# Kernel tuning notes

Measured on AMD Instinct MI355X. Metric: run time of the kernel, lower is better.

The kernel has to match this reference:

```python
import jax, jax.numpy as jnp
import numpy as np

N_HEADS = 8
LN_EPS = 1e-5
NEG = -1e9


def _layernorm(x, g, b):
    mu = jnp.mean(x, axis=-1, keepdims=True)
    var = jnp.var(x, axis=-1, keepdims=True)
    return (x - mu) * jax.lax.rsqrt(var + LN_EPS) * g + b


def setup_inputs() -> dict:
    key = jax.random.key(0)
    ks = jax.random.split(key, 16)
    B, T, D, W, L, A = 8, 256, 512, 32, 4, 6
    s = 0.02
    return {
        "feats": jax.random.normal(ks[0], (B, T, D), jnp.float32),
        "pos_embed": jax.random.normal(ks[1], (1, W, D), jnp.float32) * s,
        "Wqkv": jax.random.normal(ks[2], (L, 3 * D, D), jnp.float32) * s,
        "bqkv": jnp.zeros((L, 3 * D), jnp.float32),
        "Wo": jax.random.normal(ks[3], (L, D, D), jnp.float32) * s,
        "bo": jnp.zeros((L, D), jnp.float32),
        "ln1_g": jnp.ones((L, D), jnp.float32),
        "ln1_b": jnp.zeros((L, D), jnp.float32),
        "W1": jax.random.normal(ks[4], (L, 4 * D, D), jnp.float32) * s,
        "b1": jnp.zeros((L, 4 * D), jnp.float32),
        "W2": jax.random.normal(ks[5], (L, D, 4 * D), jnp.float32) * s,
        "b2": jnp.zeros((L, D), jnp.float32),
        "ln2_g": jnp.ones((L, D), jnp.float32),
        "ln2_b": jnp.zeros((L, D), jnp.float32),
        "Wp": jax.random.normal(ks[6], (A, D), jnp.float32) * s,
        "bp": jnp.zeros((A,), jnp.float32),
        "Wv": jax.random.normal(ks[7], (1, D), jnp.float32) * s,
        "bv": jnp.zeros((1,), jnp.float32),
    }


def reference(feats, pos_embed, Wqkv, bqkv, Wo, bo, ln1_g, ln1_b,
              W1, b1, W2, b2, ln2_g, ln2_b, Wp, bp, Wv, bv):
    B, T, D = feats.shape
    W = pos_embed.shape[1]
    L = Wqkv.shape[0]
    H = N_HEADS
    dh = D // H

    # Sliding windows for every timestep t: window slot w holds frame
    # max(t+1-W+w, 0)  (left-pad short prefixes by repeating frame 0).
    idx = jnp.maximum(jnp.arange(T)[:, None] + 1 - W + jnp.arange(W)[None, :], 0)  # (T,W)
    x = feats[:, idx, :].reshape(B * T, W, D) + pos_embed  # (B*T, W, D)

    causal = jnp.tril(jnp.ones((W, W), bool))  # additive -inf upper-tri mask

    for i in range(L):
        qkv = x @ Wqkv[i].T + bqkv[i]                     # (N,W,3D)
        q, k, v = jnp.split(qkv, 3, axis=-1)
        q = q.reshape(-1, W, H, dh).transpose(0, 2, 1, 3)
        k = k.reshape(-1, W, H, dh).transpose(0, 2, 1, 3)
        v = v.reshape(-1, W, H, dh).transpose(0, 2, 1, 3)
        scores = jnp.einsum('nhqd,nhkd->nhqk', q, k) / jnp.sqrt(jnp.float32(dh))
        scores = jnp.where(causal, scores, NEG)
        attn = jax.nn.softmax(scores, axis=-1)
        ctx = jnp.einsum('nhqk,nhkd->nhqd', attn, v)
        ctx = ctx.transpose(0, 2, 1, 3).reshape(-1, W, D)
        x = _layernorm(x + ctx @ Wo[i].T + bo[i], ln1_g[i], ln1_b[i])
        ff = jax.nn.relu(x @ W1[i].T + b1[i]) @ W2[i].T + b2[i]
        x = _layernorm(x + ff, ln2_g[i], ln2_b[i])

    token = x[:, -1, :].reshape(B, T, D)
    logits = token @ Wp.T + bp          # (B,T,A)
    values = (token @ Wv.T + bv)[..., 0]  # (B,T)
    return logits, values
```

## Files before the change

kernel.cpp:

```cpp
#include <hip/hip_runtime.h>
#include <hip/hip_bf16.h>
#include <cstdint>
#include <cstddef>

#define B_    8
#define T_    256
#define D_    512
#define W_    32
#define L_    4
#define A_    6
#define H_    8
#define DH_   64
#define NWIN  (B_*T_)
#define NTOK  (NWIN*W_)
#define FROWS 2176
#define SMALL (NWIN*D_)

typedef __hip_bfloat16 bf16;
using bf16x8 = __attribute__((ext_vector_type(8))) short;
using f32x4  = __attribute__((ext_vector_type(4))) float;
using f32x16 = __attribute__((ext_vector_type(16))) float;

#define XB_BYTES  ((size_t)NTOK * D_ * 2)
#define WQ_ELEMS  ((size_t)L_ * 3*D_*D_)
#define WO_ELEMS  ((size_t)L_ * D_*D_)
#define W1_ELEMS  ((size_t)L_ * 4*D_*D_)
#define W2_ELEMS  ((size_t)L_ * 4*D_*D_)
#define WB_BYTES  ((WQ_ELEMS + WO_ELEMS + W1_ELEMS + W2_ELEMS) * 2)
#define FB_ELEMS  ((size_t)FROWS * D_)
#define QF_ELEMS  ((size_t)FROWS * 3*D_)
#define SCR_BYTES ((size_t)NTOK * 2560 * 2)
#define TOTAL_BYTES (XB_BYTES + WB_BYTES + (FB_ELEMS + QF_ELEMS)*2 + SCR_BYTES)

static char* g_fallback = nullptr;
__attribute__((constructor)) static void alloc_fallback() {
    (void)hipMalloc((void**)&g_fallback, TOTAL_BYTES);
}

typedef __attribute__((address_space(3))) uint8_t* as3p;
typedef const __attribute__((address_space(1))) uint8_t* as1p;
__device__ __forceinline__ void gload_lds16(const void* g, void* l) {
    __builtin_amdgcn_global_load_lds((as1p)(const uint8_t*)g,
                                     (as3p)(uint32_t)(uintptr_t)l, 16, 0, 0);
}

__device__ __forceinline__ float bf2f(short s) {
    return __uint_as_float(((uint32_t)(uint16_t)s) << 16);
}
__device__ __forceinline__ short f2bf(float f) {
    return (short)__bfloat16_as_ushort(__float2bfloat16(f));
}

__global__ __launch_bounds__(256) void cvt_kernel(
    const float* __restrict__ w, bf16* __restrict__ o, int n4)
{
    int i = blockIdx.x * 256 + threadIdx.x;
    if (i >= n4) return;
    float4 f = ((const float4*)w)[i];
    bf16* d = o + (size_t)i * 4;
    d[0] = __float2bfloat16(f.x);
    d[1] = __float2bfloat16(f.y);
    d[2] = __float2bfloat16(f.z);
    d[3] = __float2bfloat16(f.w);
}

__global__ __launch_bounds__(256) void build_x_kernel(
    const float* __restrict__ feats,
    const float* __restrict__ pos,
    bf16* __restrict__ xb)
{
    int gid   = blockIdx.x * 256 + threadIdx.x;
    int token = gid >> 7;
    int c4    = (gid & 127) * 4;
    int w     = token & (W_-1);
    int n     = token >> 5;
    int t     = n & (T_-1);
    int b     = n >> 8;
    int frame = t + w - (W_-1); if (frame < 0) frame = 0;
    const float4 f = *(const float4*)(feats + ((size_t)(b*T_ + frame)*D_ + c4));
    const float4 p = *(const float4*)(pos   + ((size_t)w*D_ + c4));
    bf16* d = xb + (size_t)token*D_ + c4;
    d[0] = __float2bfloat16(f.x + p.x);
    d[1] = __float2bfloat16(f.y + p.y);
    d[2] = __float2bfloat16(f.z + p.z);
    d[3] = __float2bfloat16(f.w + p.w);
}

__global__ __launch_bounds__(256) void build_fb_kernel(
    const float* __restrict__ feats,
    const float* __restrict__ pos,
    bf16* __restrict__ fb)
{
    int gid = blockIdx.x * 256 + threadIdx.x;
    int row = gid >> 7;
    int c4  = (gid & 127) * 4;
    bf16* d = fb + (size_t)row * D_ + c4;
    float4 f;
    if (row < 2048)      f = *(const float4*)(feats + (size_t)row * D_ + c4);
    else if (row < 2080) f = *(const float4*)(pos + (size_t)(row - 2048) * D_ + c4);
    else                 f = make_float4(0.f, 0.f, 0.f, 0.f);
    d[0] = __float2bfloat16(f.x);
    d[1] = __float2bfloat16(f.y);
    d[2] = __float2bfloat16(f.z);
    d[3] = __float2bfloat16(f.w);
}

__global__ __launch_bounds__(256) void qkv_gather_kernel(
    const bf16* __restrict__ qf,
    const float* __restrict__ bq,
    bf16* __restrict__ qkv)
{
    int gid   = blockIdx.x * 256 + threadIdx.x;
    int token = gid / 192;
    int c0    = (gid % 192) * 8;
    int w     = token & (W_-1);
    int n     = token >> 5;
    int t     = n & (T_-1);
    int b     = n >> 8;
    int frame = t + w - (W_-1); if (frame < 0) frame = 0;
    const bf16x8 a = *(const bf16x8*)(qf + (size_t)(b*T_ + frame) * (3*D_) + c0);
    const bf16x8 p = *(const bf16x8*)(qf + (size_t)(2048 + w)     * (3*D_) + c0);
    bf16x8 o;
#pragma unroll
    for (int j = 0; j < 8; ++j)
        o[j] = f2bf(bf2f(a[j]) + bf2f(p[j]) + bq[c0 + j]);
    *(bf16x8*)(qkv + (size_t)token * (3*D_) + c0) = o;
}

template<bool RELU, bool BIAS, bool REMAP>
__global__ __launch_bounds__(256) void gemm_bf16(
    const bf16* __restrict__ A,
    const bf16* __restrict__ Bt,
    const float* __restrict__ bias,
    bf16* __restrict__ Cb,
    int M, int N, int K)
{
    __shared__ bf16 As[128*32];
    __shared__ bf16 Bs[128*32];

    const int tid  = threadIdx.x;
    const int lane = tid & 63;
    const int wv   = tid >> 6;

    const int gridN = N >> 7;
    const int bid   = blockIdx.x;
    int m0, n0;
    if (REMAP) {
        const int q_ = bid >> 3;
        n0 = (q_ % gridN) << 7;
        m0 = (((q_ / gridN) * 8) + (bid & 7)) << 7;
    } else {
        n0 = (bid % gridN) << 7;
        m0 = (bid / gridN) << 7;
    }

    const int wm = (wv >> 1) * 64;
    const int wn = (wv & 1) * 64;

    f32x16 acc[2][2] = {};

    const int   srow  = wv*16 + (lane >> 2);
    const int   skoff = (lane & 3) * 8;
    const bf16* ga0 = A  + (size_t)(m0 + srow)      * K + skoff;
    const bf16* ga1 = A  + (size_t)(m0 + 64 + srow) * K + skoff;
    const bf16* gb0 = Bt + (size_t)(n0 + srow)      * K + skoff;
    const bf16* gb1 = Bt + (size_t)(n0 + 64 + srow) * K + skoff;
    char* lAs = (char*)As;
    char* lBs = (char*)Bs;
    const int l0 = wv*1024 + lane*16;

    const int r32  = lane & 31;
    const int ksel = (lane >> 5) * 16;

    for (int k0 = 0; k0 < K; k0 += 32) {
        gload_lds16(ga0 + k0, lAs + l0);
        gload_lds16(ga1 + k0, lAs + l0 + 4096);
        gload_lds16(gb0 + k0, lBs + l0);
        gload_lds16(gb1 + k0, lBs + l0 + 4096);
        __syncthreads();

        bf16x8 av[2][2], bv[2][2];
#pragma unroll
        for (int i = 0; i < 2; ++i)
#pragma unroll
            for (int h = 0; h < 2; ++h) {
                av[i][h] = *(const bf16x8*)(lAs + (wm + i*32 + r32)*64 + h*32 + ksel);
                bv[i][h] = *(const bf16x8*)(lBs + (wn + i*32 + r32)*64 + h*32 + ksel);
            }
#pragma unroll
        for (int i = 0; i < 2; ++i)
#pragma unroll
            for (int j = 0; j < 2; ++j) {
                acc[i][j] = __builtin_amdgcn_mfma_f32_32x32x16_bf16(
                    av[i][0], bv[j][0], acc[i][j], 0, 0, 0);
                acc[i][j] = __builtin_amdgcn_mfma_f32_32x32x16_bf16(
                    av[i][1], bv[j][1], acc[i][j], 0, 0, 0);
            }
        __syncthreads();
    }

    const int rbase = (lane >> 5) * 4;
#pragma unroll
    for (int i = 0; i < 2; ++i) {
#pragma unroll
        for (int j = 0; j < 2; ++j) {
            const int ncol = n0 + wn + j*32 + r32;
            const float bv_ = BIAS ? bias[ncol] : 0.f;
#pragma unroll
            for (int reg = 0; reg < 16; ++reg) {
                const int mrow = m0 + wm + i*32 + (reg & 3) + 8*(reg >> 2) + rbase;
                float v = acc[i][j][reg] + bv_;
                if (RELU) v = fmaxf(v, 0.f);
                Cb[(size_t)mrow * N + ncol] = __float2bfloat16(v);
            }
        }
    }
}

template<bool RELU, bool BIAS>
__global__ __launch_bounds__(512, 2) void gemm256(
    const bf16* __restrict__ A,
    const bf16* __restrict__ Bt,
    const float* __restrict__ bias,
    bf16* __restrict__ Cb,
    int M, int N, int K)
{
    (void)M;
    __shared__ bf16 As[2][256*64];
    __shared__ bf16 Bs[2][256*64];

    const int tid  = threadIdx.x;
    const int lane = tid & 63;
    const int wv   = tid >> 6;
    const int wm   = wv >> 2;
    const int wn   = wv & 3;
    const int L    = lane & 15;
    const int qd   = lane >> 4;

    const int gridN = N >> 8;
    const int W8  = gridN << 3;
    const int bid = blockIdx.x;
    const int q_  = bid / W8;
    const int r_  = bid % W8;
    const int n0  = (r_ >> 3) << 8;
    const int m0  = ((q_ << 3) + (r_ & 7)) << 8;

    const int srow = tid >> 3;
    const int scol = ((tid & 7) ^ (srow & 7)) * 8;
    const bf16* gA = A  + (size_t)(m0 + srow) * K + scol;
    const bf16* gB = Bt + (size_t)(n0 + srow) * K + scol;
    const size_t rstep = (size_t)64 * K;
    bf16* lA = &As[0][0] + tid * 8;
    bf16* lB = &Bs[0][0] + tid * 8;

    const int physk0 = ((qd)     ^ (L & 7)) * 8;
    const int physk1 = ((4 + qd) ^ (L & 7)) * 8;
    const int aoff = (wm*128 + L) * 64;
    const int boff = (wn*64  + L) * 64;

    f32x4 acc[8][4] = {};
    bf16x8 av0[4][2], av1[4][2], bv0[2][2], bv1[2][2];

#define STAGE_A2(b, kt) do { \
    const bf16* s_ = gA + (size_t)(kt) * 64; \
    bf16* d_ = lA + (b) * 16384; \
    gload_lds16(s_,            d_); \
    gload_lds16(s_ +   rstep,  d_ + 4096); \
    gload_lds16(s_ + 2*rstep,  d_ + 8192); \
    gload_lds16(s_ + 3*rstep,  d_ + 12288); } while (0)

#define STAGE_B2(b, kt) do { \
    const bf16* s_ = gB + (size_t)(kt) * 64; \
    bf16* d_ = lB + (b) * 16384; \
    gload_lds16(s_,            d_); \
    gload_lds16(s_ +   rstep,  d_ + 4096); \
    gload_lds16(s_ + 2*rstep,  d_ + 8192); \
    gload_lds16(s_ + 3*rstep,  d_ + 12288); } while (0)

#define LDA_(dst, b, qm) do { \
    const bf16* pa_ = &As[b][aoff + (qm)*4096]; \
    _Pragma("unroll") \
    for (int mr_ = 0; mr_ < 4; ++mr_) { \
        dst[mr_][0] = *(const bf16x8*)(pa_ + mr_*1024 + physk0); \
        dst[mr_][1] = *(const bf16x8*)(pa_ + mr_*1024 + physk1); } } while (0)

#define LDB_(dst, b, qn) do { \
    const bf16* pb_ = &Bs[b][boff + (qn)*2048]; \
    _Pragma("unroll") \
    for (int nr_ = 0; nr_ < 2; ++nr_) { \
        dst[nr_][0] = *(const bf16x8*)(pb_ + nr_*1024 + physk0); \
        dst[nr_][1] = *(const bf16x8*)(pb_ + nr_*1024 + physk1); } } while (0)

#define MMA_(qm, qn, av, bv) do { \
    _Pragma("unroll") \
    for (int mr_ = 0; mr_ < 4; ++mr_) \
    _Pragma("unroll") \
    for (int nr_ = 0; nr_ < 2; ++nr_) { \
        f32x4 c_ = acc[(qm)*4+mr_][(qn)*2+nr_]; \
        c_ = __builtin_amdgcn_mfma_f32_16x16x32_bf16(av[mr_][0], bv[nr_][0], c_, 0, 0, 0); \
        c_ = __builtin_amdgcn_mfma_f32_16x16x32_bf16(av[mr_][1], bv[nr_][1], c_, 0, 0, 0); \
        acc[(qm)*4+mr_][(qn)*2+nr_] = c_; } } while (0)

#define BAR_ __builtin_amdgcn_s_barrier()
#define LGKM0_ do { asm volatile("s_waitcnt lgkmcnt(0)" ::: "memory"); \
                    __builtin_amdgcn_sched_barrier(0); } while (0)

#define TILE_(b, kt2) do { \
     \
    LDA_(av0, b, 0); LDB_(bv0, b, 0); \
    BAR_; LGKM0_; \
    __builtin_amdgcn_s_setprio(1); MMA_(0, 0, av0, bv0); __builtin_amdgcn_s_setprio(0); \
    BAR_; \
     \
    LDB_(bv1, b, 1); \
    BAR_; LGKM0_; \
    __builtin_amdgcn_s_setprio(1); MMA_(0, 1, av0, bv1); __builtin_amdgcn_s_setprio(0); \
    BAR_; \
     \
    LDA_(av1, b, 1); \
    STAGE_B2(b, kt2); \
    BAR_; LGKM0_; \
    __builtin_amdgcn_s_setprio(1); MMA_(1, 1, av1, bv1); __builtin_amdgcn_s_setprio(0); \
    BAR_; \
     \
    STAGE_A2(b, kt2); \
    __builtin_amdgcn_s_setprio(1); MMA_(1, 0, av1, bv0); __builtin_amdgcn_s_setprio(0); \
    asm volatile("s_waitcnt vmcnt(8)" ::: "memory"); \
    BAR_; } while (0)

    const int nkt = K >> 6;

    STAGE_B2(0, 0); STAGE_A2(0, 0);
    STAGE_B2(1, 1); STAGE_A2(1, 1);
    asm volatile("s_waitcnt vmcnt(8)" ::: "memory");
    BAR_;

    for (int u = 0; u < nkt; u += 2) {
        int k2 = u + 2; if (k2 >= nkt) k2 -= nkt;
        int k3 = u + 3; if (k3 >= nkt) k3 -= nkt;
        TILE_(0, k2);
        TILE_(1, k3);
    }

    asm volatile("s_waitcnt vmcnt(0)" ::: "memory");

#pragma unroll
    for (int mr = 0; mr < 8; ++mr) {
        const int row = m0 + wm*128 + mr*16 + qd*4;
#pragma unroll
        for (int nr = 0; nr < 4; ++nr) {
            const int col = n0 + wn*64 + nr*16 + L;
            const float bb = BIAS ? bias[col] : 0.f;
            bf16* cp = Cb + (size_t)row * N + col;
#pragma unroll
            for (int rg = 0; rg < 4; ++rg) {
                float v = acc[mr][nr][rg] + bb;
                if (RELU) v = fmaxf(v, 0.f);
                cp[(size_t)rg * N] = __float2bfloat16(v);
            }
        }
    }

#undef STAGE_A2
#undef STAGE_B2
#undef LDA_
#undef LDB_
#undef MMA_
#undef BAR_
#undef LGKM0_
#undef TILE_
}

__global__ __launch_bounds__(256) void lnres_kernel(
    const bf16* __restrict__ y,
    const bf16* __restrict__ xin,
    bf16* __restrict__ xout,
    const float* __restrict__ g,
    const float* __restrict__ b,
    int xin_stride)
{
    const int wave  = threadIdx.x >> 6;
    const int lane  = threadIdx.x & 63;
    const int token = blockIdx.x * 4 + wave;
    const int c0    = lane * 8;

    const bf16* yr = y    + (size_t)token * D_ + c0;
    const bf16* xr = xin  + (size_t)token * xin_stride + c0;
    bf16*       xo = xout + (size_t)token * D_ + c0;

    bf16x8 ty = *(const bf16x8*)yr;
    bf16x8 tx = *(const bf16x8*)xr;

    float v[8];
    float s1 = 0.f, s2 = 0.f;
#pragma unroll
    for (int j = 0; j < 8; ++j) {
        v[j] = bf2f(ty[j]) + bf2f(tx[j]);
        s1 += v[j]; s2 += v[j]*v[j];
    }
#pragma unroll
    for (int mask = 1; mask < 64; mask <<= 1) {
        s1 += __shfl_xor(s1, mask);
        s2 += __shfl_xor(s2, mask);
    }
    const float mu = s1 * (1.f / D_);
    float var = s2 * (1.f / D_) - mu * mu;
    if (var < 0.f) var = 0.f;
    const float rs = rsqrtf(var + 1e-5f);

    const float4 g0 = *(const float4*)(g + c0);
    const float4 g1 = *(const float4*)(g + c0 + 4);
    const float4 b0 = *(const float4*)(b + c0);
    const float4 b1 = *(const float4*)(b + c0 + 4);
    const float gg[8] = {g0.x,g0.y,g0.z,g0.w,g1.x,g1.y,g1.z,g1.w};
    const float bb[8] = {b0.x,b0.y,b0.z,b0.w,b1.x,b1.y,b1.z,b1.w};

    bf16x8 o;
#pragma unroll
    for (int j = 0; j < 8; ++j) {
        float t = (v[j] - mu) * rs * gg[j] + bb[j];
        o[j] = f2bf(t);
    }
    *(bf16x8*)xo = o;
}

__global__ __launch_bounds__(256) void attn_mfma(
    const bf16* __restrict__ qkv,
    bf16* __restrict__ ctx)
{
    __shared__ short Pb[4][32*32];

    const int tid  = threadIdx.x;
    const int lane = tid & 63;
    const int wv   = tid >> 6;
    const int pair = blockIdx.x * 4 + wv;
    const int win  = pair >> 3;
    const int h    = pair & 7;

    const int quad = lane >> 4;
    const int col  = lane & 15;

    const bf16* base = qkv + (size_t)win * W_ * (3*D_) + h * DH_;

    bf16x8 bvv[4];
    {
        const short* vbase = (const short*)(base + 2*D_);
#pragma unroll
        for (int ntd = 0; ntd < 4; ++ntd)
#pragma unroll
            for (int jj = 0; jj < 8; ++jj)
                bvv[ntd][jj] = vbase[(size_t)(quad*8 + jj) * (3*D_) + ntd*16 + col];
    }

    bf16x8 aq[2][2], bk[2][2];
#pragma unroll
    for (int mt = 0; mt < 2; ++mt)
#pragma unroll
        for (int kq = 0; kq < 2; ++kq)
            aq[mt][kq] = *(const bf16x8*)(base + (size_t)(mt*16 + col) * (3*D_)
                                          + kq*32 + quad*8);
#pragma unroll
    for (int nt = 0; nt < 2; ++nt)
#pragma unroll
        for (int kq = 0; kq < 2; ++kq)
            bk[nt][kq] = *(const bf16x8*)(base + D_ + (size_t)(nt*16 + col) * (3*D_)
                                          + kq*32 + quad*8);

    f32x4 S[2][2] = {};
#pragma unroll
    for (int mt = 0; mt < 2; ++mt)
#pragma unroll
        for (int nt = 0; nt < 2; ++nt) {
            S[mt][nt] = __builtin_amdgcn_mfma_f32_16x16x32_bf16(
                aq[mt][0], bk[nt][0], S[mt][nt], 0, 0, 0);
            S[mt][nt] = __builtin_amdgcn_mfma_f32_16x16x32_bf16(
                aq[mt][1], bk[nt][1], S[mt][nt], 0, 0, 0);
        }

    short* P = Pb[wv];
#pragma unroll
    for (int mt = 0; mt < 2; ++mt) {
#pragma unroll
        for (int reg = 0; reg < 4; ++reg) {
            const int row = mt*16 + quad*4 + reg;
            float v0 = (col      <= row) ? S[mt][0][reg] * 0.125f : -1e30f;
            float v1 = (16 + col <= row) ? S[mt][1][reg] * 0.125f : -1e30f;
            float mx = fmaxf(v0, v1);
#pragma unroll
            for (int m = 1; m < 16; m <<= 1) mx = fmaxf(mx, __shfl_xor(mx, m));
            float e0 = __expf(v0 - mx);
            float e1 = __expf(v1 - mx);
            float sm = e0 + e1;
#pragma unroll
            for (int m = 1; m < 16; m <<= 1) sm += __shfl_xor(sm, m);
            float inv = 1.f / sm;
            P[row*32 + col]      = f2bf(e0 * inv);
            P[row*32 + 16 + col] = f2bf(e1 * inv);
        }
    }

    bf16* cb = ctx + (size_t)win * W_ * D_ + h * DH_;
#pragma unroll
    for (int mt = 0; mt < 2; ++mt) {
        bf16x8 ap = *(const bf16x8*)(P + (mt*16 + col)*32 + quad*8);
#pragma unroll
        for (int ntd = 0; ntd < 4; ++ntd) {
            f32x4 O = {};
            O = __builtin_amdgcn_mfma_f32_16x16x32_bf16(ap, bvv[ntd], O, 0, 0, 0);
#pragma unroll
            for (int reg = 0; reg < 4; ++reg) {
                const int row = mt*16 + quad*4 + reg;
                cb[(size_t)row * D_ + ntd*16 + col] = __float2bfloat16(O[reg]);
            }
        }
    }
}

__global__ __launch_bounds__(256) void attn_last(
    const bf16* __restrict__ qkv,
    bf16* __restrict__ ctxl)
{
    __shared__ float Ps[4][32];

    const int wv   = threadIdx.x >> 6;
    const int lane = threadIdx.x & 63;
    const int pair = blockIdx.x * 4 + wv;
    const int win  = pair >> 3;
    const int h    = pair & 7;

    const bf16* base = qkv + (size_t)win * W_ * (3*D_) + h * DH_;
    const short* qrow = (const short*)(base + (size_t)(W_-1) * (3*D_));

    const int k    = lane & 31;
    const int half = lane >> 5;
    const short* krow = (const short*)(base + D_ + (size_t)k * (3*D_) + half*32);

    float s = 0.f;
    const bf16x8* q8 = (const bf16x8*)(qrow + half*32);
    const bf16x8* k8 = (const bf16x8*)krow;
#pragma unroll
    for (int c = 0; c < 4; ++c) {
        bf16x8 qa = q8[c], kb = k8[c];
#pragma unroll
        for (int j = 0; j < 8; ++j) s += bf2f(qa[j]) * bf2f(kb[j]);
    }
    s += __shfl_xor(s, 32);
    s *= 0.125f;

    float mx = s;
#pragma unroll
    for (int m = 1; m < 32; m <<= 1) mx = fmaxf(mx, __shfl_xor(mx, m));
    float e = __expf(s - mx);
    float sum = e;
#pragma unroll
    for (int m = 1; m < 32; m <<= 1) sum += __shfl_xor(sum, m);
    if (half == 0) Ps[wv][k] = e / sum;
    __syncthreads();

    const short* vbase = (const short*)(base + 2*D_);
    float o = 0.f;
#pragma unroll
    for (int kk = 0; kk < 32; ++kk)
        o += Ps[wv][kk] * bf2f(vbase[(size_t)kk * (3*D_) + lane]);

    ctxl[(size_t)win * D_ + h * DH_ + lane] = __float2bfloat16(o);
}

__global__ __launch_bounds__(64) void head_kernel(
    const bf16* __restrict__ xq,
    const float* __restrict__ Wp, const float* __restrict__ bp,
    const float* __restrict__ Wv, const float* __restrict__ bv,
    float* __restrict__ out)
{
    const int n    = blockIdx.x;
    const int lane = threadIdx.x;
    const bf16* row = xq + (size_t)n * D_;
    float t[8];
#pragma unroll
    for (int j = 0; j < 8; ++j) t[j] = bf2f(*(const short*)(row + lane + j*64));

    for (int a = 0; a < A_ + 1; ++a) {
        const float* w = (a < A_) ? (Wp + (size_t)a * D_) : Wv;
        float d = 0.f;
#pragma unroll
        for (int j = 0; j < 8; ++j) d += t[j] * w[lane + j*64];
#pragma unroll
        for (int off = 32; off > 0; off >>= 1) d += __shfl_down(d, off);
        if (lane == 0) {
            if (a < A_) out[(size_t)n*A_ + a] = d + bp[a];
            else        out[(size_t)NWIN*A_ + n] = d + bv[0];
        }
    }
}

extern "C" void kernel_launch(void* const* d_in, const int* in_sizes, int n_in,
                              void* d_out, int out_size, void* d_ws, size_t ws_size,
                              hipStream_t stream) {
    const float* feats = (const float*)d_in[0];
    const float* pos   = (const float*)d_in[1];
    const float* Wqkv  = (const float*)d_in[2];
    const float* bqkv  = (const float*)d_in[3];
    const float* Wo    = (const float*)d_in[4];
    const float* bo    = (const float*)d_in[5];
    const float* ln1g  = (const float*)d_in[6];
    const float* ln1b  = (const float*)d_in[7];
    const float* W1    = (const float*)d_in[8];
    const float* b1    = (const float*)d_in[9];
    const float* W2    = (const float*)d_in[10];
    const float* b2    = (const float*)d_in[11];
    const float* ln2g  = (const float*)d_in[12];
    const float* ln2b  = (const float*)d_in[13];
    const float* Wp    = (const float*)d_in[14];
    const float* bp    = (const float*)d_in[15];
    const float* Wv    = (const float*)d_in[16];
    const float* bv    = (const float*)d_in[17];
    float* out = (float*)d_out;

    char* basep = (ws_size >= TOTAL_BYTES) ? (char*)d_ws : g_fallback;

    bf16*  xb   = (bf16*)basep;
    bf16*  wq_b = (bf16*)(basep + XB_BYTES);
    bf16*  wo_b = wq_b + WQ_ELEMS;
    bf16*  w1_b = wo_b + WO_ELEMS;
    bf16*  w2_b = w1_b + W1_ELEMS;
    bf16*  fb   = w2_b + W2_ELEMS;
    bf16*  qf   = fb + FB_ELEMS;
    bf16*  scr  = qf + QF_ELEMS;
    bf16*  qkv_s = scr;
    bf16*  ctx_s = scr + (size_t)NTOK * (3*D_);
    bf16*  h_s   = scr;
    bf16*  y_s   = scr + (size_t)NTOK * 2048;
    bf16*  ctxl = ctx_s;
    bf16*  ysm  = ctx_s + (size_t)SMALL;
    bf16*  hsm  = ctx_s + (size_t)2*SMALL;
    bf16*  xq   = ctx_s + (size_t)6*SMALL;

    cvt_kernel<<<(WQ_ELEMS/4 + 255)/256, 256, 0, stream>>>(Wqkv, wq_b, WQ_ELEMS/4);
    cvt_kernel<<<(WO_ELEMS/4 + 255)/256, 256, 0, stream>>>(Wo,   wo_b, WO_ELEMS/4);
    cvt_kernel<<<(W1_ELEMS/4 + 255)/256, 256, 0, stream>>>(W1,   w1_b, W1_ELEMS/4);
    cvt_kernel<<<(W2_ELEMS/4 + 255)/256, 256, 0, stream>>>(W2,   w2_b, W2_ELEMS/4);

    build_x_kernel<<<NTOK * (D_/4) / 256, 256, 0, stream>>>(feats, pos, xb);
    build_fb_kernel<<<FROWS * (D_/4) / 256, 256, 0, stream>>>(feats, pos, fb);

    const int GM2 = NTOK / 256;

    for (int i = 0; i < L_; ++i) {
        const bf16*  wq_i = wq_b + (size_t)i * 3*D_*D_;
        const float* bq_i = bqkv + (size_t)i * 3*D_;
        const bf16*  wo_i = wo_b + (size_t)i * D_*D_;
        const float* bo_i = bo   + (size_t)i * D_;
        const bf16*  w1_i = w1_b + (size_t)i * 4*D_*D_;
        const float* b1_i = b1   + (size_t)i * 4*D_;
        const bf16*  w2_i = w2_b + (size_t)i * 4*D_*D_;
        const float* b2_i = b2   + (size_t)i * D_;

        if (i == 0) {
            gemm_bf16<false,false,false><<<(FROWS/128) * (3*D_/128), 256, 0, stream>>>(
                fb, wq_i, nullptr, qf, FROWS, 3*D_, D_);
            qkv_gather_kernel<<<NTOK * 192 / 256, 256, 0, stream>>>(qf, bq_i, qkv_s);
        } else {
            gemm256<false,true><<<GM2 * (3*D_/256), 512, 0, stream>>>(
                xb, wq_i, bq_i, qkv_s, NTOK, 3*D_, D_);
        }

        if (i < L_-1) {
            attn_mfma<<<NWIN * H_ / 4, 256, 0, stream>>>(qkv_s, ctx_s);
            gemm256<false,true><<<GM2 * (D_/256), 512, 0, stream>>>(
                ctx_s, wo_i, bo_i, y_s, NTOK, D_, D_);
            lnres_kernel<<<NTOK/4, 256, 0, stream>>>(
                y_s, xb, xb, ln1g + (size_t)i*D_, ln1b + (size_t)i*D_, D_);
            gemm256<true,true><<<GM2 * (4*D_/256), 512, 0, stream>>>(
                xb, w1_i, b1_i, h_s, NTOK, 4*D_, D_);
            gemm256<false,true><<<GM2 * (D_/256), 512, 0, stream>>>(
                h_s, w2_i, b2_i, y_s, NTOK, D_, 4*D_);
            lnres_kernel<<<NTOK/4, 256, 0, stream>>>(
                y_s, xb, xb, ln2g + (size_t)i*D_, ln2b + (size_t)i*D_, D_);
        } else {
            attn_last<<<NWIN * H_ / 4, 256, 0, stream>>>(qkv_s, ctxl);
            gemm_bf16<false,true,false><<<(NWIN/128) * (D_/128), 256, 0, stream>>>(
                ctxl, wo_i, bo_i, ysm, NWIN, D_, D_);
            lnres_kernel<<<NWIN/4, 256, 0, stream>>>(
                ysm, xb + (size_t)(W_-1)*D_, xq,
                ln1g + (size_t)i*D_, ln1b + (size_t)i*D_, W_*D_);
            gemm_bf16<true,true,false><<<(NWIN/128) * (4*D_/128), 256, 0, stream>>>(
                xq, w1_i, b1_i, hsm, NWIN, 4*D_, D_);
            gemm_bf16<false,true,false><<<(NWIN/128) * (D_/128), 256, 0, stream>>>(
                hsm, w2_i, b2_i, ysm, NWIN, D_, 4*D_);
            lnres_kernel<<<NWIN/4, 256, 0, stream>>>(
                ysm, xq, xq, ln2g + (size_t)i*D_, ln2b + (size_t)i*D_, D_);
        }
    }

    head_kernel<<<NWIN, 64, 0, stream>>>(xq, Wp, bp, Wv, bv, out);
}
```

Baseline: 2.101 ms.

## Replace 256x256 GEMM tile with 256x128 triple-buffered K=32 pipeline

Swaps the large-GEMM kernel from a 256x256 output tile, double-buffered with K=64 stages, to a 256x128 tile with K=32 stages and a three-deep LDS ring. The launch bound is raised to 4 blocks per CU and the grid doubles. The aim is more occupancy and latency hiding from the smaller LDS footprint and deeper prefetch. The cost is lower arithmetic intensity per tile, more global traffic for A, and more barriers per unit of K.

Result: slower. 2.228 ms (+6.0%).

```diff
diff --git a/kernel.cpp b/kernel.cpp
--- a/kernel.cpp
+++ b/kernel.cpp
@@ -218,7 +218,7 @@
 }
 
 template<bool RELU, bool BIAS>
-__global__ __launch_bounds__(512, 2) void gemm256(
+__global__ __launch_bounds__(512, 4) void gemm256h(
     const bf16* __restrict__ A,
     const bf16* __restrict__ Bt,
     const float* __restrict__ bias,
@@ -226,127 +226,103 @@
     int M, int N, int K)
 {
     (void)M;
-    __shared__ bf16 As[2][256*64];
-    __shared__ bf16 Bs[2][256*64];
+    __shared__ bf16 As[3][256*32];
+    __shared__ bf16 Bs[3][128*32];
 
     const int tid  = threadIdx.x;
     const int lane = tid & 63;
     const int wv   = tid >> 6;
-    const int wm   = wv >> 2;
-    const int wn   = wv & 3;
+    const int wm   = wv >> 1;
+    const int wn   = wv & 1;
     const int L    = lane & 15;
     const int qd   = lane >> 4;
 
-    const int gridN = N >> 8;
+    const int gridN = N >> 7;
     const int W8  = gridN << 3;
     const int bid = blockIdx.x;
     const int q_  = bid / W8;
     const int r_  = bid % W8;
-    const int n0  = (r_ >> 3) << 8;
+    const int n0  = (r_ >> 3) << 7;
     const int m0  = ((q_ << 3) + (r_ & 7)) << 8;
 
-    const int srow = tid >> 3;
-    const int scol = ((tid & 7) ^ (srow & 7)) * 8;
-    const bf16* gA = A  + (size_t)(m0 + srow) * K + scol;
-    const bf16* gB = Bt + (size_t)(n0 + srow) * K + scol;
-    const size_t rstep = (size_t)64 * K;
+    const int srow = tid >> 2;
+    const int slog = (tid & 3) ^ ((srow >> 1) & 3);
+    const bf16* gA = A  + (size_t)(m0 + srow) * K + slog * 8;
+    const bf16* gB = Bt + (size_t)(n0 + srow) * K + slog * 8;
+    const size_t rstep = (size_t)128 * K;
     bf16* lA = &As[0][0] + tid * 8;
     bf16* lB = &Bs[0][0] + tid * 8;
 
-    const int physk0 = ((qd)     ^ (L & 7)) * 8;
-    const int physk1 = ((4 + qd) ^ (L & 7)) * 8;
-    const int aoff = (wm*128 + L) * 64;
-    const int boff = (wn*64  + L) * 64;
-
-    f32x4 acc[8][4] = {};
-    bf16x8 av0[4][2], av1[4][2], bv0[2][2], bv1[2][2];
-
-#define STAGE_A2(b, kt) do { \
-    const bf16* s_ = gA + (size_t)(kt) * 64; \
-    bf16* d_ = lA + (b) * 16384; \
-    gload_lds16(s_,            d_); \
-    gload_lds16(s_ +   rstep,  d_ + 4096); \
-    gload_lds16(s_ + 2*rstep,  d_ + 8192); \
-    gload_lds16(s_ + 3*rstep,  d_ + 12288); } while (0)
-
-#define STAGE_B2(b, kt) do { \
-    const bf16* s_ = gB + (size_t)(kt) * 64; \
-    bf16* d_ = lB + (b) * 16384; \
-    gload_lds16(s_,            d_); \
-    gload_lds16(s_ +   rstep,  d_ + 4096); \
-    gload_lds16(s_ + 2*rstep,  d_ + 8192); \
-    gload_lds16(s_ + 3*rstep,  d_ + 12288); } while (0)
-
-#define LDA_(dst, b, qm) do { \
-    const bf16* pa_ = &As[b][aoff + (qm)*4096]; \
-    _Pragma("unroll") \
-    for (int mr_ = 0; mr_ < 4; ++mr_) { \
-        dst[mr_][0] = *(const bf16x8*)(pa_ + mr_*1024 + physk0); \
-        dst[mr_][1] = *(const bf16x8*)(pa_ + mr_*1024 + physk1); } } while (0)
-
-#define LDB_(dst, b, qn) do { \
-    const bf16* pb_ = &Bs[b][boff + (qn)*2048]; \
-    _Pragma("unroll") \
-    for (int nr_ = 0; nr_ < 2; ++nr_) { \
-        dst[nr_][0] = *(const bf16x8*)(pb_ + nr_*1024 + physk0); \
-        dst[nr_][1] = *(const bf16x8*)(pb_ + nr_*1024 + physk1); } } while (0)
-
-#define MMA_(qm, qn, av, bv) do { \
-    _Pragma("unroll") \
-    for (int mr_ = 0; mr_ < 4; ++mr_) \
-    _Pragma("unroll") \
-    for (int nr_ = 0; nr_ < 2; ++nr_) { \
-        f32x4 c_ = acc[(qm)*4+mr_][(qn)*2+nr_]; \
-        c_ = __builtin_amdgcn_mfma_f32_16x16x32_bf16(av[mr_][0], bv[nr_][0], c_, 0, 0, 0); \
-        c_ = __builtin_amdgcn_mfma_f32_16x16x32_bf16(av[mr_][1], bv[nr_][1], c_, 0, 0, 0); \
-        acc[(qm)*4+mr_][(qn)*2+nr_] = c_; } } while (0)
+    const int kchunk = (qd ^ ((L >> 1) & 3)) * 8;
+    const int aoff = (wm*64 + L) * 32 + kchunk;
+    const int boff = (wn*64 + L) * 32 + kchunk;
+
+    f32x4 acc[4][4] = {};
+    bf16x8 av01[2], av23[2], bv[4];
+
+#define STAGE_(buf, kt) do { \
+    const bf16* sa_ = gA + (size_t)(kt) * 32; \
+    gload_lds16(sa_,          lA + (buf) * 8192); \
+    gload_lds16(sa_ + rstep,  lA + (buf) * 8192 + 4096); \
+    gload_lds16(gB + (size_t)(kt) * 32, lB + (buf) * 4096); } while (0)
 
 #define BAR_ __builtin_amdgcn_s_barrier()
 #define LGKM0_ do { asm volatile("s_waitcnt lgkmcnt(0)" ::: "memory"); \
                     __builtin_amdgcn_sched_barrier(0); } while (0)
 
-#define TILE_(b, kt2) do { \
-     \
-    LDA_(av0, b, 0); LDB_(bv0, b, 0); \
-    BAR_; LGKM0_; \
-    __builtin_amdgcn_s_setprio(1); MMA_(0, 0, av0, bv0); __builtin_amdgcn_s_setprio(0); \
-    BAR_; \
-     \
-    LDB_(bv1, b, 1); \
-    BAR_; LGKM0_; \
-    __builtin_amdgcn_s_setprio(1); MMA_(0, 1, av0, bv1); __builtin_amdgcn_s_setprio(0); \
-    BAR_; \
-     \
-    LDA_(av1, b, 1); \
-    STAGE_B2(b, kt2); \
-    BAR_; LGKM0_; \
-    __builtin_amdgcn_s_setprio(1); MMA_(1, 1, av1, bv1); __builtin_amdgcn_s_setprio(0); \
-    BAR_; \
-     \
-    STAGE_A2(b, kt2); \
-    __builtin_amdgcn_s_setprio(1); MMA_(1, 0, av1, bv0); __builtin_amdgcn_s_setprio(0); \
-    asm volatile("s_waitcnt vmcnt(8)" ::: "memory"); \
-    BAR_; } while (0)
-
-    const int nkt = K >> 6;
-
-    STAGE_B2(0, 0); STAGE_A2(0, 0);
-    STAGE_B2(1, 1); STAGE_A2(1, 1);
-    asm volatile("s_waitcnt vmcnt(8)" ::: "memory");
+    const int nt = K >> 5;
+
+    STAGE_(0, 0);
+    STAGE_(1, 1);
+    asm volatile("s_waitcnt vmcnt(3)" ::: "memory");
     BAR_;
 
-    for (int u = 0; u < nkt; u += 2) {
-        int k2 = u + 2; if (k2 >= nkt) k2 -= nkt;
-        int k3 = u + 3; if (k3 >= nkt) k3 -= nkt;
-        TILE_(0, k2);
-        TILE_(1, k3);
+    int b0 = 0;
+    for (int t = 0; t < nt; ++t) {
+        const int tgt = (b0 + 2 >= 3) ? b0 - 1 : b0 + 2;
+        const int kt2 = (t + 2 < nt) ? t + 2 : t;
+        const bf16* pa = &As[b0][aoff];
+        const bf16* pb = &Bs[b0][boff];
+
+        STAGE_(tgt, kt2);
+        av01[0] = *(const bf16x8*)(pa);
+        av01[1] = *(const bf16x8*)(pa + 512);
+#pragma unroll
+        for (int nr = 0; nr < 4; ++nr)
+            bv[nr] = *(const bf16x8*)(pb + nr*512);
+        BAR_; LGKM0_;
+        __builtin_amdgcn_s_setprio(1);
+#pragma unroll
+        for (int mr = 0; mr < 2; ++mr)
+#pragma unroll
+            for (int nr = 0; nr < 4; ++nr)
+                acc[mr][nr] = __builtin_amdgcn_mfma_f32_16x16x32_bf16(
+                    av01[mr], bv[nr], acc[mr][nr], 0, 0, 0);
+        __builtin_amdgcn_s_setprio(0);
+        BAR_;
+
+        av23[0] = *(const bf16x8*)(pa + 1024);
+        av23[1] = *(const bf16x8*)(pa + 1536);
+        BAR_; LGKM0_;
+        __builtin_amdgcn_s_setprio(1);
+#pragma unroll
+        for (int mr = 0; mr < 2; ++mr)
+#pragma unroll
+            for (int nr = 0; nr < 4; ++nr)
+                acc[2+mr][nr] = __builtin_amdgcn_mfma_f32_16x16x32_bf16(
+                    av23[mr], bv[nr], acc[2+mr][nr], 0, 0, 0);
+        __builtin_amdgcn_s_setprio(0);
+        asm volatile("s_waitcnt vmcnt(3)" ::: "memory");
+        BAR_;
+
+        b0 = (b0 == 2) ? 0 : b0 + 1;
     }
 
     asm volatile("s_waitcnt vmcnt(0)" ::: "memory");
 
 #pragma unroll
-    for (int mr = 0; mr < 8; ++mr) {
-        const int row = m0 + wm*128 + mr*16 + qd*4;
+    for (int mr = 0; mr < 4; ++mr) {
+        const int row = m0 + wm*64 + mr*16 + qd*4;
 #pragma unroll
         for (int nr = 0; nr < 4; ++nr) {
             const int col = n0 + wn*64 + nr*16 + L;
@@ -361,14 +337,9 @@
         }
     }
 
-#undef STAGE_A2
-#undef STAGE_B2
-#undef LDA_
-#undef LDB_
-#undef MMA_
+#undef STAGE_
 #undef BAR_
 #undef LGKM0_
-#undef TILE_
 }
 
 __global__ __launch_bounds__(256) void lnres_kernel(
@@ -660,19 +631,19 @@
                 fb, wq_i, nullptr, qf, FROWS, 3*D_, D_);
             qkv_gather_kernel<<<NTOK * 192 / 256, 256, 0, stream>>>(qf, bq_i, qkv_s);
         } else {
-            gemm256<false,true><<<GM2 * (3*D_/256), 512, 0, stream>>>(
+            gemm256h<false,true><<<GM2 * (3*D_/128), 512, 0, stream>>>(
                 xb, wq_i, bq_i, qkv_s, NTOK, 3*D_, D_);
         }
 
         if (i < L_-1) {
             attn_mfma<<<NWIN * H_ / 4, 256, 0, stream>>>(qkv_s, ctx_s);
-            gemm256<false,true><<<GM2 * (D_/256), 512, 0, stream>>>(
+            gemm256h<false,true><<<GM2 * (D_/128), 512, 0, stream>>>(
                 ctx_s, wo_i, bo_i, y_s, NTOK, D_, D_);
             lnres_kernel<<<NTOK/4, 256, 0, stream>>>(
                 y_s, xb, xb, ln1g + (size_t)i*D_, ln1b + (size_t)i*D_, D_);
-            gemm256<true,true><<<GM2 * (4*D_/256), 512, 0, stream>>>(
+            gemm256h<true,true><<<GM2 * (4*D_/128), 512, 0, stream>>>(
                 xb, w1_i, b1_i, h_s, NTOK, 4*D_, D_);
-            gemm256<false,true><<<GM2 * (D_/256), 512, 0, stream>>>(
+            gemm256h<false,true><<<GM2 * (D_/128), 512, 0, stream>>>(
                 h_s, w2_i, b2_i, y_s, NTOK, D_, 4*D_);
             lnres_kernel<<<NTOK/4, 256, 0, stream>>>(
                 y_s, xb, xb, ln2g + (size_t)i*D_, ln2b + (size_t)i*D_, D_);
```

## Fuse layer-0 QKV gather into attention; compute only last-row Q in final layer

Applied to the files above, without the earlier changes.

Layer 0 no longer materialises the full gathered QKV tensor. The attention kernel reads the per-frame projections directly and adds a precomputed position-plus-bias table on the fly. In the last layer only K and V are projected for all tokens, and Q is projected just for the final window slot via a small GEMM on a sliced copy of x. This cuts a large memory write/read and about a third of the last layer's QKV GEMM, at the cost of scattered gathered loads inside attention.

Result: faster. 2.056 ms (-2.1%).

```diff
diff --git a/kernel.cpp b/kernel.cpp
--- a/kernel.cpp
+++ b/kernel.cpp
@@ -29,8 +29,9 @@
 #define WB_BYTES  ((WQ_ELEMS + WO_ELEMS + W1_ELEMS + W2_ELEMS) * 2)
 #define FB_ELEMS  ((size_t)FROWS * D_)
 #define QF_ELEMS  ((size_t)FROWS * 3*D_)
+#define PPB_ELEMS ((size_t)W_ * 3*D_)
 #define SCR_BYTES ((size_t)NTOK * 2560 * 2)
-#define TOTAL_BYTES (XB_BYTES + WB_BYTES + (FB_ELEMS + QF_ELEMS)*2 + SCR_BYTES)
+#define TOTAL_BYTES (XB_BYTES + WB_BYTES + (FB_ELEMS + QF_ELEMS)*2 + PPB_ELEMS*4 + SCR_BYTES)
 
 static char* g_fallback = nullptr;
 __attribute__((constructor)) static void alloc_fallback() {
@@ -105,26 +106,23 @@
     d[3] = __float2bfloat16(f.w);
 }
 
-__global__ __launch_bounds__(256) void qkv_gather_kernel(
+__global__ __launch_bounds__(256) void build_ppb_kernel(
     const bf16* __restrict__ qf,
     const float* __restrict__ bq,
-    bf16* __restrict__ qkv)
-{
-    int gid   = blockIdx.x * 256 + threadIdx.x;
-    int token = gid / 192;
-    int c0    = (gid % 192) * 8;
-    int w     = token & (W_-1);
-    int n     = token >> 5;
-    int t     = n & (T_-1);
-    int b     = n >> 8;
-    int frame = t + w - (W_-1); if (frame < 0) frame = 0;
-    const bf16x8 a = *(const bf16x8*)(qf + (size_t)(b*T_ + frame) * (3*D_) + c0);
-    const bf16x8 p = *(const bf16x8*)(qf + (size_t)(2048 + w)     * (3*D_) + c0);
-    bf16x8 o;
-#pragma unroll
-    for (int j = 0; j < 8; ++j)
-        o[j] = f2bf(bf2f(a[j]) + bf2f(p[j]) + bq[c0 + j]);
-    *(bf16x8*)(qkv + (size_t)token * (3*D_) + c0) = o;
+    float* __restrict__ ppb)
+{
+    int gid = blockIdx.x * 256 + threadIdx.x;
+    int w = gid / (3*D_), c = gid % (3*D_);
+    ppb[gid] = bf2f(*(const short*)(qf + (size_t)(2048 + w) * (3*D_) + c)) + bq[c];
+}
+
+__global__ __launch_bounds__(256) void slice31_kernel(
+    const bf16* __restrict__ xb, bf16* __restrict__ xg)
+{
+    int gid = blockIdx.x * 256 + threadIdx.x;
+    int n = gid >> 6, c0 = (gid & 63) * 8;
+    *(bf16x8*)(xg + (size_t)n*D_ + c0) =
+        *(const bf16x8*)(xb + (size_t)(n*W_ + (W_-1))*D_ + c0);
 }
 
 template<bool RELU, bool BIAS, bool REMAP>
@@ -516,8 +514,111 @@
     }
 }
 
-__global__ __launch_bounds__(256) void attn_last(
-    const bf16* __restrict__ qkv,
+__global__ __launch_bounds__(256) void attn_mfma0(
+    const bf16* __restrict__ qf,
+    const float* __restrict__ ppb,
+    bf16* __restrict__ ctx)
+{
+    __shared__ short Pb[4][32*32];
+
+    const int tid  = threadIdx.x;
+    const int lane = tid & 63;
+    const int wv   = tid >> 6;
+    const int pair = blockIdx.x * 4 + wv;
+    const int win  = pair >> 3;
+    const int h    = pair & 7;
+
+    const int quad = lane >> 4;
+    const int col  = lane & 15;
+    const int bb_  = win >> 8;
+    const int tt_  = win & (T_-1);
+
+#define FR_(w) ((size_t)(bb_*T_ + ((tt_ + (w) - (W_-1)) > 0 ? (tt_ + (w) - (W_-1)) : 0)) * (3*D_))
+
+    bf16x8 bvv[4];
+#pragma unroll
+    for (int ntd = 0; ntd < 4; ++ntd)
+#pragma unroll
+        for (int jj = 0; jj < 8; ++jj) {
+            const int w2 = quad*8 + jj;
+            const int c  = 2*D_ + h*DH_ + ntd*16 + col;
+            bvv[ntd][jj] = f2bf(bf2f(*(const short*)(qf + FR_(w2) + c))
+                                + ppb[w2*(3*D_) + c]);
+        }
+
+    bf16x8 aq[2][2], bk[2][2];
+#pragma unroll
+    for (int mt = 0; mt < 2; ++mt)
+#pragma unroll
+        for (int kq = 0; kq < 2; ++kq) {
+            const int w  = mt*16 + col;
+            const size_t fro = FR_(w);
+            const int cq = h*DH_ + kq*32 + quad*8;
+            const bf16x8 a = *(const bf16x8*)(qf + fro + cq);
+            const bf16x8 k = *(const bf16x8*)(qf + fro + D_ + cq);
+            const float* pq = ppb + w*(3*D_) + cq;
+            const float* pk = pq + D_;
+#pragma unroll
+            for (int j = 0; j < 8; ++j) {
+                aq[mt][kq][j] = f2bf(bf2f(a[j]) + pq[j]);
+                bk[mt][kq][j] = f2bf(bf2f(k[j]) + pk[j]);
+            }
+        }
+#undef FR_
+
+    f32x4 S[2][2] = {};
+#pragma unroll
+    for (int mt = 0; mt < 2; ++mt)
+#pragma unroll
+        for (int nt = 0; nt < 2; ++nt) {
+            S[mt][nt] = __builtin_amdgcn_mfma_f32_16x16x32_bf16(
+                aq[mt][0], bk[nt][0], S[mt][nt], 0, 0, 0);
+            S[mt][nt] = __builtin_amdgcn_mfma_f32_16x16x32_bf16(
+                aq[mt][1], bk[nt][1], S[mt][nt], 0, 0, 0);
+        }
+
+    short* P = Pb[wv];
+#pragma unroll
+    for (int mt = 0; mt < 2; ++mt) {
+#pragma unroll
+        for (int reg = 0; reg < 4; ++reg) {
+            const int row = mt*16 + quad*4 + reg;
+            float v0 = (col      <= row) ? S[mt][0][reg] * 0.125f : -1e30f;
+            float v1 = (16 + col <= row) ? S[mt][1][reg] * 0.125f : -1e30f;
+            float mx = fmaxf(v0, v1);
+#pragma unroll
+            for (int m = 1; m < 16; m <<= 1) mx = fmaxf(mx, __shfl_xor(mx, m));
+            float e0 = __expf(v0 - mx);
+            float e1 = __expf(v1 - mx);
+            float sm = e0 + e1;
+#pragma unroll
+            for (int m = 1; m < 16; m <<= 1) sm += __shfl_xor(sm, m);
+            float inv = 1.f / sm;
+            P[row*32 + col]      = f2bf(e0 * inv);
+            P[row*32 + 16 + col] = f2bf(e1 * inv);
+        }
+    }
+
+    bf16* cb = ctx + (size_t)win * W_ * D_ + h * DH_;
+#pragma unroll
+    for (int mt = 0; mt < 2; ++mt) {
+        bf16x8 ap = *(const bf16x8*)(P + (mt*16 + col)*32 + quad*8);
+#pragma unroll
+        for (int ntd = 0; ntd < 4; ++ntd) {
+            f32x4 O = {};
+            O = __builtin_amdgcn_mfma_f32_16x16x32_bf16(ap, bvv[ntd], O, 0, 0, 0);
+#pragma unroll
+            for (int reg = 0; reg < 4; ++reg) {
+                const int row = mt*16 + quad*4 + reg;
+                cb[(size_t)row * D_ + ntd*16 + col] = __float2bfloat16(O[reg]);
+            }
+        }
+    }
+}
+
+__global__ __launch_bounds__(256) void attn_last2(
+    const bf16* __restrict__ kv,
+    const bf16* __restrict__ q31,
     bf16* __restrict__ ctxl)
 {
     __shared__ float Ps[4][32];
@@ -528,21 +629,21 @@
     const int win  = pair >> 3;
     const int h    = pair & 7;
 
-    const bf16* base = qkv + (size_t)win * W_ * (3*D_) + h * DH_;
-    const short* qrow = (const short*)(base + (size_t)(W_-1) * (3*D_));
+    const bf16* kb   = kv + (size_t)win * W_ * 1024 + h * DH_;
+    const short* qrow = (const short*)(q31 + (size_t)win * D_ + h * DH_);
 
     const int k    = lane & 31;
     const int half = lane >> 5;
-    const short* krow = (const short*)(base + D_ + (size_t)k * (3*D_) + half*32);
+    const short* krow = (const short*)(kb + (size_t)k * 1024 + half*32);
 
     float s = 0.f;
     const bf16x8* q8 = (const bf16x8*)(qrow + half*32);
     const bf16x8* k8 = (const bf16x8*)krow;
 #pragma unroll
     for (int c = 0; c < 4; ++c) {
-        bf16x8 qa = q8[c], kb = k8[c];
-#pragma unroll
-        for (int j = 0; j < 8; ++j) s += bf2f(qa[j]) * bf2f(kb[j]);
+        bf16x8 qa = q8[c], kb_ = k8[c];
+#pragma unroll
+        for (int j = 0; j < 8; ++j) s += bf2f(qa[j]) * bf2f(kb_[j]);
     }
     s += __shfl_xor(s, 32);
     s *= 0.125f;
@@ -557,11 +658,11 @@
     if (half == 0) Ps[wv][k] = e / sum;
     __syncthreads();
 
-    const short* vbase = (const short*)(base + 2*D_);
+    const short* vb = (const short*)(kb + 512);
     float o = 0.f;
 #pragma unroll
     for (int kk = 0; kk < 32; ++kk)
-        o += Ps[wv][kk] * bf2f(vbase[(size_t)kk * (3*D_) + lane]);
+        o += Ps[wv][kk] * bf2f(vb[(size_t)kk * 1024 + lane]);
 
     ctxl[(size_t)win * D_ + h * DH_ + lane] = __float2bfloat16(o);
 }
@@ -625,8 +726,10 @@
     bf16*  w2_b = w1_b + W1_ELEMS;
     bf16*  fb   = w2_b + W2_ELEMS;
     bf16*  qf   = fb + FB_ELEMS;
-    bf16*  scr  = qf + QF_ELEMS;
+    float* ppb  = (float*)(qf + QF_ELEMS);
+    bf16*  scr  = (bf16*)(ppb + PPB_ELEMS);
     bf16*  qkv_s = scr;
+    bf16*  kv_s  = scr;
     bf16*  ctx_s = scr + (size_t)NTOK * (3*D_);
     bf16*  h_s   = scr;
     bf16*  y_s   = scr + (size_t)NTOK * 2048;
@@ -634,6 +737,8 @@
     bf16*  ysm  = ctx_s + (size_t)SMALL;
     bf16*  hsm  = ctx_s + (size_t)2*SMALL;
     bf16*  xq   = ctx_s + (size_t)6*SMALL;
+    bf16*  xg   = ctx_s + (size_t)8*SMALL;
+    bf16*  q31  = ctx_s + (size_t)9*SMALL;
 
     cvt_kernel<<<(WQ_ELEMS/4 + 255)/256, 256, 0, stream>>>(Wqkv, wq_b, WQ_ELEMS/4);
     cvt_kernel<<<(WO_ELEMS/4 + 255)/256, 256, 0, stream>>>(Wo,   wo_b, WO_ELEMS/4);
@@ -658,14 +763,15 @@
         if (i == 0) {
             gemm_bf16<false,false,false><<<(FROWS/128) * (3*D_/128), 256, 0, stream>>>(
                 fb, wq_i, nullptr, qf, FROWS, 3*D_, D_);
-            qkv_gather_kernel<<<NTOK * 192 / 256, 256, 0, stream>>>(qf, bq_i, qkv_s);
-        } else {
+            build_ppb_kernel<<<W_*(3*D_)/256, 256, 0, stream>>>(qf, bq_i, ppb);
+            attn_mfma0<<<NWIN * H_ / 4, 256, 0, stream>>>(qf, ppb, ctx_s);
+        } else if (i < L_-1) {
             gemm256<false,true><<<GM2 * (3*D_/256), 512, 0, stream>>>(
                 xb, wq_i, bq_i, qkv_s, NTOK, 3*D_, D_);
+            attn_mfma<<<NWIN * H_ / 4, 256, 0, stream>>>(qkv_s, ctx_s);
         }
 
         if (i < L_-1) {
-            attn_mfma<<<NWIN * H_ / 4, 256, 0, stream>>>(qkv_s, ctx_s);
             gemm256<false,true><<<GM2 * (D_/256), 512, 0, stream>>>(
                 ctx_s, wo_i, bo_i, y_s, NTOK, D_, D_);
             lnres_kernel<<<NTOK/4, 256, 0, stream>>>(
@@ -677,12 +783,17 @@
             lnres_kernel<<<NTOK/4, 256, 0, stream>>>(
                 y_s, xb, xb, ln2g + (size_t)i*D_, ln2b + (size_t)i*D_, D_);
         } else {
-            attn_last<<<NWIN * H_ / 4, 256, 0, stream>>>(qkv_s, ctxl);
+            gemm256<false,true><<<GM2 * (1024/256), 512, 0, stream>>>(
+                xb, wq_i + (size_t)D_*D_, bq_i + D_, kv_s, NTOK, 2*D_, D_);
+            slice31_kernel<<<NWIN*64/256, 256, 0, stream>>>(xb, xg);
+            gemm_bf16<false,true,false><<<(NWIN/128) * (D_/128), 256, 0, stream>>>(
+                xg, wq_i, bq_i, q31, NWIN, D_, D_);
+            attn_last2<<<NWIN * H_ / 4, 256, 0, stream>>>(kv_s, q31, ctxl);
             gemm_bf16<false,true,false><<<(NWIN/128) * (D_/128), 256, 0, stream>>>(
                 ctxl, wo_i, bo_i, ysm, NWIN, D_, D_);
             lnres_kernel<<<NWIN/4, 256, 0, stream>>>(
-                ysm, xb + (size_t)(W_-1)*D_, xq,
-                ln1g + (size_t)i*D_, ln1b + (size_t)i*D_, W_*D_);
+                ysm, xg, xq,
+                ln1g + (size_t)i*D_, ln1b + (size_t)i*D_, D_);
             gemm_bf16<true,true,false><<<(NWIN/128) * (4*D_/128), 256, 0, stream>>>(
                 xq, w1_i, b1_i, hsm, NWIN, 4*D_, D_);
             gemm_bf16<false,true,false><<<(NWIN/128) * (D_/128), 256, 0, stream>>>(
```
